# Performance work log

Hardware: AMD Instinct MI355X
Metric: run time of the kernel (lower is better)

Reference implementation:

```python
import jax, jax.numpy as jnp
import numpy as np


def fwht(x):
    """Fast Walsh-Hadamard transform along axis 1 of a (B, n, D) array.
    Unnormalized, matches the torch butterfly: (a+b, a-b) per stage."""
    B, n, D = x.shape
    h = 1
    y = x
    while h < n:  # log2(n) static stages
        # group axis-1 into blocks of 2*h: (B, n//(2h), 2, h, D)
        y = y.reshape(B, n // (2 * h), 2, h, D)
        a = y[:, :, 0]
        b = y[:, :, 1]
        y = jnp.stack((a + b, a - b), axis=2).reshape(B, n, D)
        h *= 2
    return y


def setup_inputs() -> dict:
    key = jax.random.key(0)
    x = jax.random.normal(key, (64, 1024, 512), dtype=jnp.float32)
    return {"x": x}


def reference(x):
    return fwht(x)
```

## Files before the change

### kernel.cpp

```cpp
#include <hip/hip_runtime.h>


constexpr int NB = 64;
constexpr int NR = 1024;
constexpr int ND = 512;
constexpr int DC = 16;
constexpr int TPB = 256;

__global__ __launch_bounds__(TPB, 2)
void fwht_kernel(const float* __restrict__ x, float* __restrict__ y) {
    __shared__ float lds[NR * DC];

    const int tid = threadIdx.x;
    const int b     = blockIdx.x & 63;
    const int dg    = blockIdx.x >> 6;
    const int dbase = dg * DC;

    const int g = tid >> 2;
    const int w = tid & 3;
    const float* src = x + ((size_t)b * NR + (size_t)g * 16) * ND + dbase + w * 4;

    float4 v[16];
#pragma unroll
    for (int j = 0; j < 16; ++j)
        v[j] = *reinterpret_cast<const float4*>(src + (size_t)j * ND);

#pragma unroll
    for (int hb = 1; hb < 16; hb <<= 1) {
#pragma unroll
        for (int j = 0; j < 16; ++j) {
            if ((j & hb) == 0) {
                const int k = j | hb;
                float4 a = v[j], bb = v[k];
                v[j] = make_float4(a.x + bb.x, a.y + bb.y, a.z + bb.z, a.w + bb.w);
                v[k] = make_float4(a.x - bb.x, a.y - bb.y, a.z - bb.z, a.w - bb.w);
            }
        }
    }

    {
        const int p0  = g & 1;
        const int S   = (g >> 1) & 15;
        const int Shi = S & 12, Slo = S & 3;
        float* lp = lds + g * 256 + ((w * 4) ^ Shi);
#pragma unroll
        for (int j = 0; j < 16; ++j) {
            float* row = lp + ((j ^ p0) * 16);
            row[0 ^ Slo] = v[j].x;
            row[1 ^ Slo] = v[j].y;
            row[2 ^ Slo] = v[j].z;
            row[3 ^ Slo] = v[j].w;
        }
    }
    __syncthreads();

    const int j2 = tid >> 4;
    const int c  = tid & 15;
    float u[64];
#pragma unroll
    for (int i = 0; i < 64; ++i) {
        const int addr = i * 256 + ((j2 ^ (i & 1)) * 16) + (c ^ ((i >> 1) & 15));
        u[i] = lds[addr];
    }

#pragma unroll
    for (int hb = 1; hb < 64; hb <<= 1) {
#pragma unroll
        for (int i = 0; i < 64; ++i) {
            if ((i & hb) == 0) {
                const int k = i | hb;
                float a = u[i], bb = u[k];
                u[i] = a + bb;
                u[k] = a - bb;
            }
        }
    }

    float* dst = y + ((size_t)b * NR + j2) * ND + dbase + c;
#pragma unroll
    for (int i = 0; i < 64; ++i)
        dst[(size_t)(i * 16) * ND] = u[i];
}

extern "C" void kernel_launch(void* const* d_in, const int* in_sizes, int n_in,
                              void* d_out, int out_size, void* d_ws, size_t ws_size,
                              hipStream_t stream) {
    const float* x = (const float*)d_in[0];
    float* y = (float*)d_out;
    dim3 grid(NB * (ND / DC));
    fwht_kernel<<<grid, TPB, 0, stream>>>(x, y);
}
```

Before: 259.7 us.

## Persistent blocks with prefetched next tile and LDS-staged float4 output stores

Shrinks the grid to 512 persistent blocks, each processing four D-chunk tiles in a loop. The global loads for the next tile are issued before the current tile is computed, so load latency overlaps with compute. The output now goes back through swizzled LDS so it can be written as coalesced float4 rows instead of scattered scalar stores. The cost is extra LDS round trips, more barriers (raw s_barrier asm) and higher register pressure from the prefetch buffer, which may reduce occupancy.

Measured after the change: 259.1 us. Within noise of the previous version (-0.3%).

```diff
diff --git a/kernel.cpp b/kernel.cpp
--- a/kernel.cpp
+++ b/kernel.cpp
@@ -6,80 +6,118 @@
 constexpr int ND = 512;
 constexpr int DC = 16;
 constexpr int TPB = 256;
+constexpr int GRID = 512;
+constexpr int TPT = (NB * (ND / DC)) / GRID;
+
+#define BAR() asm volatile("s_waitcnt lgkmcnt(0)\n\ts_barrier" ::: "memory")
 
 __global__ __launch_bounds__(TPB, 2)
 void fwht_kernel(const float* __restrict__ x, float* __restrict__ y) {
     __shared__ float lds[NR * DC];
 
     const int tid = threadIdx.x;
-    const int b     = blockIdx.x & 63;
-    const int dg    = blockIdx.x >> 6;
-    const int dbase = dg * DC;
+    const int pid = blockIdx.x;
+    const int b   = pid & 63;
+    const int dg0 = pid >> 6;
 
-    const int g = tid >> 2;
-    const int w = tid & 3;
-    const float* src = x + ((size_t)b * NR + (size_t)g * 16) * ND + dbase + w * 4;
+    const int g  = tid >> 2;
+    const int w  = tid & 3;
+    const int j2 = tid >> 4;
+    const int c  = tid & 15;
+
+    const size_t rowA = ((size_t)b * NR + (size_t)g * 16) * ND + (size_t)(w * 4);
 
     float4 v[16];
+    {
+        const float* src = x + rowA + dg0 * DC;
 #pragma unroll
-    for (int j = 0; j < 16; ++j)
-        v[j] = *reinterpret_cast<const float4*>(src + (size_t)j * ND);
-
-#pragma unroll
-    for (int hb = 1; hb < 16; hb <<= 1) {
-#pragma unroll
-        for (int j = 0; j < 16; ++j) {
-            if ((j & hb) == 0) {
-                const int k = j | hb;
-                float4 a = v[j], bb = v[k];
-                v[j] = make_float4(a.x + bb.x, a.y + bb.y, a.z + bb.z, a.w + bb.w);
-                v[k] = make_float4(a.x - bb.x, a.y - bb.y, a.z - bb.z, a.w - bb.w);
-            }
-        }
-    }
-
-    {
-        const int p0  = g & 1;
-        const int S   = (g >> 1) & 15;
-        const int Shi = S & 12, Slo = S & 3;
-        float* lp = lds + g * 256 + ((w * 4) ^ Shi);
-#pragma unroll
-        for (int j = 0; j < 16; ++j) {
-            float* row = lp + ((j ^ p0) * 16);
-            row[0 ^ Slo] = v[j].x;
-            row[1 ^ Slo] = v[j].y;
-            row[2 ^ Slo] = v[j].z;
-            row[3 ^ Slo] = v[j].w;
-        }
-    }
-    __syncthreads();
-
-    const int j2 = tid >> 4;
-    const int c  = tid & 15;
-    float u[64];
-#pragma unroll
-    for (int i = 0; i < 64; ++i) {
-        const int addr = i * 256 + ((j2 ^ (i & 1)) * 16) + (c ^ ((i >> 1) & 15));
-        u[i] = lds[addr];
+        for (int j = 0; j < 16; ++j)
+            v[j] = *reinterpret_cast<const float4*>(src + (size_t)j * ND);
     }
 
 #pragma unroll
-    for (int hb = 1; hb < 64; hb <<= 1) {
+    for (int t = 0; t < TPT; ++t) {
+        const int dbase = (dg0 + 8 * t) * DC;
+
+        float4 vn[16];
+        if (t < TPT - 1) {
+            const float* srcn = x + rowA + (dbase + 8 * DC);
+#pragma unroll
+            for (int j = 0; j < 16; ++j)
+                vn[j] = *reinterpret_cast<const float4*>(srcn + (size_t)j * ND);
+        }
+
+#pragma unroll
+        for (int hb = 1; hb < 16; hb <<= 1) {
+#pragma unroll
+            for (int j = 0; j < 16; ++j) {
+                if ((j & hb) == 0) {
+                    const int k = j | hb;
+                    float4 a = v[j], bb = v[k];
+                    v[j] = make_float4(a.x + bb.x, a.y + bb.y, a.z + bb.z, a.w + bb.w);
+                    v[k] = make_float4(a.x - bb.x, a.y - bb.y, a.z - bb.z, a.w - bb.w);
+                }
+            }
+        }
+
+        {
+            const int p0  = g & 1;
+            const int S   = (g >> 1) & 15;
+            const int Shi = S & 12, Slo = S & 3;
+            float* lp = lds + g * 256 + ((w * 4) ^ Shi);
+#pragma unroll
+            for (int j = 0; j < 16; ++j) {
+                float* row = lp + ((j ^ p0) * 16);
+                row[0 ^ Slo] = v[j].x;
+                row[1 ^ Slo] = v[j].y;
+                row[2 ^ Slo] = v[j].z;
+                row[3 ^ Slo] = v[j].w;
+            }
+        }
+        BAR();
+
+        float u[64];
 #pragma unroll
         for (int i = 0; i < 64; ++i) {
-            if ((i & hb) == 0) {
-                const int k = i | hb;
-                float a = u[i], bb = u[k];
-                u[i] = a + bb;
-                u[k] = a - bb;
+            const int addr = i * 256 + ((j2 ^ (i & 1)) * 16) + (c ^ ((i >> 1) & 15));
+            u[i] = lds[addr];
+        }
+
+#pragma unroll
+        for (int hb = 1; hb < 64; hb <<= 1) {
+#pragma unroll
+            for (int i = 0; i < 64; ++i) {
+                if ((i & hb) == 0) {
+                    const int k = i | hb;
+                    float a = u[i], bb = u[k];
+                    u[i] = a + bb;
+                    u[k] = a - bb;
+                }
             }
         }
+        BAR();
+
+#pragma unroll
+        for (int i = 0; i < 64; ++i)
+            lds[256 * i + 16 * j2 + (c ^ ((i & 3) << 2))] = u[i];
+        BAR();
+
+        {
+            float* dst = y + rowA + dbase;
+            const int cg = (w ^ (g & 3)) << 2;
+#pragma unroll
+            for (int j = 0; j < 16; ++j) {
+                float4 wv = *reinterpret_cast<const float4*>(&lds[(16 * g + j) * 16 + cg]);
+                *reinterpret_cast<float4*>(dst + (size_t)j * ND) = wv;
+            }
+        }
+        BAR();
+
+        if (t < TPT - 1) {
+#pragma unroll
+            for (int j = 0; j < 16; ++j) v[j] = vn[j];
+        }
     }
-
-    float* dst = y + ((size_t)b * NR + j2) * ND + dbase + c;
-#pragma unroll
-    for (int i = 0; i < 64; ++i)
-        dst[(size_t)(i * 16) * ND] = u[i];
 }
 
 extern "C" void kernel_launch(void* const* d_in, const int* in_sizes, int n_in,
@@ -87,6 +125,5 @@
                               hipStream_t stream) {
     const float* x = (const float*)d_in[0];
     float* y = (float*)d_out;
-    dim3 grid(NB * (ND / DC));
-    fwht_kernel<<<grid, TPB, 0, stream>>>(x, y);
+    fwht_kernel<<<dim3(GRID), dim3(TPB), 0, stream>>>(x, y);
 }
```

## Split FWHT into two global-memory passes without shared-memory transpose

Applied to the files above, without the earlier changes.

Replaces the single kernel that used an LDS transpose with two kernels. The first does a 32-point butterfly over contiguous row groups and writes to the output. The second does a strided 32-point butterfly in place on the output. This removes the shared-memory staging, the sync and the narrow 16-column tiles in favour of wide coalesced float2 rows and higher occupancy, at the cost of doubling global memory traffic and adding a second launch.

After: 318.5 us. 22.6% more time.

```diff
diff --git a/kernel.cpp b/kernel.cpp
--- a/kernel.cpp
+++ b/kernel.cpp
@@ -4,82 +4,64 @@
 constexpr int NB = 64;
 constexpr int NR = 1024;
 constexpr int ND = 512;
-constexpr int DC = 16;
 constexpr int TPB = 256;
 
-__global__ __launch_bounds__(TPB, 2)
-void fwht_kernel(const float* __restrict__ x, float* __restrict__ y) {
-    __shared__ float lds[NR * DC];
+__global__ __launch_bounds__(TPB, 4)
+void fwht_lo(const float* __restrict__ x, float* __restrict__ y) {
+    const int b = blockIdx.x & 63;
+    const int q = blockIdx.x >> 6;
+    const size_t base = ((size_t)b * NR + (size_t)q * 32) * ND + threadIdx.x * 2;
 
-    const int tid = threadIdx.x;
-    const int b     = blockIdx.x & 63;
-    const int dg    = blockIdx.x >> 6;
-    const int dbase = dg * DC;
-
-    const int g = tid >> 2;
-    const int w = tid & 3;
-    const float* src = x + ((size_t)b * NR + (size_t)g * 16) * ND + dbase + w * 4;
-
-    float4 v[16];
+    float2 u[32];
 #pragma unroll
-    for (int j = 0; j < 16; ++j)
-        v[j] = *reinterpret_cast<const float4*>(src + (size_t)j * ND);
+    for (int r = 0; r < 32; ++r)
+        u[r] = *reinterpret_cast<const float2*>(x + base + (size_t)r * ND);
 
 #pragma unroll
-    for (int hb = 1; hb < 16; hb <<= 1) {
+    for (int hb = 1; hb < 32; hb <<= 1) {
 #pragma unroll
-        for (int j = 0; j < 16; ++j) {
-            if ((j & hb) == 0) {
-                const int k = j | hb;
-                float4 a = v[j], bb = v[k];
-                v[j] = make_float4(a.x + bb.x, a.y + bb.y, a.z + bb.z, a.w + bb.w);
-                v[k] = make_float4(a.x - bb.x, a.y - bb.y, a.z - bb.z, a.w - bb.w);
+        for (int r = 0; r < 32; ++r) {
+            if ((r & hb) == 0) {
+                const int k = r | hb;
+                const float2 a = u[r], c = u[k];
+                u[r] = make_float2(a.x + c.x, a.y + c.y);
+                u[k] = make_float2(a.x - c.x, a.y - c.y);
             }
         }
     }
 
-    {
-        const int p0  = g & 1;
-        const int S   = (g >> 1) & 15;
-        const int Shi = S & 12, Slo = S & 3;
-        float* lp = lds + g * 256 + ((w * 4) ^ Shi);
 #pragma unroll
-        for (int j = 0; j < 16; ++j) {
-            float* row = lp + ((j ^ p0) * 16);
-            row[0 ^ Slo] = v[j].x;
-            row[1 ^ Slo] = v[j].y;
-            row[2 ^ Slo] = v[j].z;
-            row[3 ^ Slo] = v[j].w;
-        }
-    }
-    __syncthreads();
+    for (int r = 0; r < 32; ++r)
+        *reinterpret_cast<float2*>(y + base + (size_t)r * ND) = u[r];
+}
 
-    const int j2 = tid >> 4;
-    const int c  = tid & 15;
-    float u[64];
+__global__ __launch_bounds__(TPB, 4)
+void fwht_hi(float* __restrict__ y) {
+    const int b = blockIdx.x & 63;
+    const int q = blockIdx.x >> 6;
+    const size_t base = ((size_t)b * NR + (size_t)q) * ND + threadIdx.x * 2;
+
+    float2 u[32];
 #pragma unroll
-    for (int i = 0; i < 64; ++i) {
-        const int addr = i * 256 + ((j2 ^ (i & 1)) * 16) + (c ^ ((i >> 1) & 15));
-        u[i] = lds[addr];
-    }
+    for (int i = 0; i < 32; ++i)
+        u[i] = *reinterpret_cast<const float2*>(y + base + (size_t)(i * 32) * ND);
 
 #pragma unroll
-    for (int hb = 1; hb < 64; hb <<= 1) {
+    for (int hb = 1; hb < 32; hb <<= 1) {
 #pragma unroll
-        for (int i = 0; i < 64; ++i) {
+        for (int i = 0; i < 32; ++i) {
             if ((i & hb) == 0) {
                 const int k = i | hb;
-                float a = u[i], bb = u[k];
-                u[i] = a + bb;
-                u[k] = a - bb;
+                const float2 a = u[i], c = u[k];
+                u[i] = make_float2(a.x + c.x, a.y + c.y);
+                u[k] = make_float2(a.x - c.x, a.y - c.y);
             }
         }
     }
 
-    float* dst = y + ((size_t)b * NR + j2) * ND + dbase + c;
 #pragma unroll
-    for (int i = 0; i < 64; ++i)
-        dst[(size_t)(i * 16) * ND] = u[i];
+    for (int i = 0; i < 32; ++i)
+        *reinterpret_cast<float2*>(y + base + (size_t)(i * 32) * ND) = u[i];
 }
 
 extern "C" void kernel_launch(void* const* d_in, const int* in_sizes, int n_in,
@@ -87,6 +69,7 @@
                               hipStream_t stream) {
     const float* x = (const float*)d_in[0];
     float* y = (float*)d_out;
-    dim3 grid(NB * (ND / DC));
-    fwht_kernel<<<grid, TPB, 0, stream>>>(x, y);
+    const int grid = NB * (NR / 32);
+    fwht_lo<<<dim3(grid), dim3(TPB), 0, stream>>>(x, y);
+    fwht_hi<<<dim3(grid), dim3(TPB), 0, stream>>>(y);
 }
```
